# Kernel optimization log

Hardware: AMD Instinct MI355X
Metric: run time of the kernel (lower is better)

The kernel has to match this reference:

```python
import jax, jax.numpy as jnp
import numpy as np

B, H_, W_, C, HEADS, WS, SR = 4, 56, 56, 256, 8, 3, 4
HD = C // HEADS
N = H_ * W_
LL = WS * WS
PH, PW = H_ // SR, W_ // SR
PL = PH * PW
K_TAB = 2048


def _unfold3(x, H, W):
    # x: (B, C, H, W) -> (B, C, 9, H*W); matches torch nn.Unfold(kernel_size=3, padding=1)
    xp = jnp.pad(x, ((0, 0), (0, 0), (1, 1), (1, 1)))
    pats = jnp.stack([xp[:, :, i:i + H, j:j + W] for i in range(3) for j in range(3)], axis=2)
    return pats.reshape(x.shape[0], x.shape[1], 9, H * W)


def _l2n(x):
    # torch F.normalize(dim=-1) with eps=1e-12
    return x / jnp.maximum(jnp.linalg.norm(x, axis=-1, keepdims=True), 1e-12)


def setup_inputs() -> dict:
    key = jax.random.key(0)
    ks = jax.random.split(key, 24)
    x = jax.random.normal(ks[0], (B, N, C), jnp.float32)
    # padding mask from unfold of ones image (True where window element falls outside)
    ones = np.zeros((H_ + 2, W_ + 2), np.float32)
    ones[1:-1, 1:-1] = 1.0
    pats = np.stack([ones[i:i + H_, j:j + W_] for i in range(3) for j in range(3)], 0).reshape(9, N)
    padding_mask = jnp.asarray((pats == 0).T)  # (N, 9) bool
    local_valid = LL - padding_mask.sum(-1)
    seq_length_scale = jnp.log(local_valid.astype(jnp.float32) + PL)[:, None]  # (N,1)
    relative_pos_index = jax.random.randint(ks[1], (N * PL,), 0, K_TAB)
    relative_coords_table = jax.random.uniform(ks[2], (K_TAB, 2), jnp.float32, -1.0, 1.0)
    w = lambda k, shape: jax.random.normal(k, shape, jnp.float32) * 0.02
    inp = dict(
        x=x, H=H_, W=W_,
        relative_pos_index=relative_pos_index,
        relative_coords_table=relative_coords_table,
        seq_length_scale=seq_length_scale,
        padding_mask=padding_mask,
        q_w=w(ks[3], (C, C)), q_b=jnp.zeros((C,), jnp.float32),
        kv_w=w(ks[4], (2 * C, C)), kv_b=jnp.zeros((2 * C,), jnp.float32),
        sr_w=w(ks[5], (C, C)), sr_b=jnp.zeros((C,), jnp.float32),
        norm_g=jnp.ones((C,), jnp.float32), norm_b=jnp.zeros((C,), jnp.float32),
        cpb1_w=w(ks[6], (512, 2)), cpb1_b=jnp.zeros((512,), jnp.float32),
        cpb2_w=w(ks[7], (HEADS, 512)), cpb2_b=jnp.zeros((HEADS,), jnp.float32),
        temperature=jnp.log(jnp.exp(jnp.ones((HEADS, 1, 1), jnp.float32) / 0.24) - 1.0),
        query_embedding=w(ks[8], (HEADS, 1, HD)),
        rel_pos_bias_local=jax.random.normal(ks[9], (HEADS, LL), jnp.float32) * 0.0004,
        learnable_tokens=w(ks[10], (HEADS, HD, LL)),
        learnable_bias=jnp.zeros((HEADS, 1, LL), jnp.float32),
        proj_w=w(ks[11], (C, C)), proj_b=jnp.zeros((C,), jnp.float32),
    )
    return inp


def reference(x, H, W, relative_pos_index, relative_coords_table, seq_length_scale,
              padding_mask, q_w, q_b, kv_w, kv_b, sr_w, sr_b, norm_g, norm_b,
              cpb1_w, cpb1_b, cpb2_w, cpb2_b, temperature, query_embedding,
              rel_pos_bias_local, learnable_tokens, learnable_bias, proj_w, proj_b):
    Bsz, n, Cd = x.shape
    h, hd, ll = HEADS, HD, LL
    pH, pW = H // SR, W // SR
    pL = pH * pW
    # ----- queries -----
    q = (x @ q_w.T + q_b).reshape(Bsz, n, h, hd).transpose(0, 2, 1, 3)  # (B,h,N,d)
    q_norm = _l2n(q)
    q_scaled = (q_norm + query_embedding) * jax.nn.softplus(temperature) * seq_length_scale
    # ----- local branch: unfolded window KV -----
    kv = x @ kv_w.T + kv_b  # (B,N,2C)
    k_loc, v_loc = jnp.split(kv, 2, axis=-1)
    k_loc = _l2n(k_loc.reshape(Bsz, n, h, hd)).reshape(Bsz, n, Cd)
    kv_img = jnp.concatenate([k_loc, v_loc], -1).transpose(0, 2, 1).reshape(Bsz, 2 * Cd, H, W)
    pats = _unfold3(kv_img, H, W).reshape(Bsz, 2 * h, hd, ll, n).transpose(0, 1, 4, 2, 3)  # (B,2h,N,d,ll)
    k_local, v_local = jnp.split(pats, 2, axis=1)
    attn_local = jnp.einsum('bhnd,bhndl->bhnl', q_scaled, k_local) + rel_pos_bias_local[:, None, :]
    attn_local = jnp.where(padding_mask, -jnp.inf, attn_local)
    # ----- global branch: 1x1 conv -> GELU -> avg pool -> LN -> KV -----
    x_img = x.transpose(0, 2, 1).reshape(Bsz, Cd, H, W)
    x_sr = jax.nn.gelu(jnp.einsum('oc,bchw->bohw', sr_w, x_img) + sr_b[None, :, None, None], approximate=False)
    x_pool = x_sr.reshape(Bsz, Cd, pH, SR, pW, SR).mean(axis=(3, 5)).reshape(Bsz, Cd, pL).transpose(0, 2, 1)
    mu = x_pool.mean(-1, keepdims=True)
    var = x_pool.var(-1, keepdims=True)
    x_pool = (x_pool - mu) / jnp.sqrt(var + 1e-5) * norm_g + norm_b
    kvp = (x_pool @ kv_w.T + kv_b).reshape(Bsz, pL, 2 * h, hd).transpose(0, 2, 1, 3)
    k_pool, v_pool = jnp.split(kvp, 2, axis=1)  # each (B,h,pL,d)
    # CPB-MLP relative position bias (interpolate is identity since test==trained resolution)
    tab = jax.nn.relu(relative_coords_table @ cpb1_w.T + cpb1_b) @ cpb2_w.T + cpb2_b  # (K,h)
    pool_bias = tab.T[:, relative_pos_index].reshape(h, n, pL)
    attn_pool = jnp.einsum('bhnd,bhmd->bhnm', q_scaled, _l2n(k_pool)) + pool_bias
    # ----- joint softmax over [local | pool] -----
    attn = jax.nn.softmax(jnp.concatenate([attn_local, attn_pool], axis=-1), axis=-1)
    a_loc, a_pool = attn[..., :ll], attn[..., ll:]
    w_loc = jnp.einsum('bhnd,hdl->bhnl', q_norm, learnable_tokens) + learnable_bias + a_loc
    x_local = jnp.einsum('bhnl,bhndl->bhnd', w_loc, v_local)
    x_glob = jnp.einsum('bhnm,bhmd->bhnd', a_pool, v_pool)
    out = (x_local + x_glob).transpose(0, 2, 1, 3).reshape(Bsz, n, Cd)
    return out @ proj_w.T + proj_b
```

## Files before the change

### kernel.cpp

```cpp
#include <hip/hip_runtime.h>
#include <hip/hip_bf16.h>
#include <math.h>

#define Bn   4
#define Hh   56
#define Wn   56
#define Cn   256
#define NHn  8
#define HDn  32
#define Nn   3136
#define LLn  9
#define PLn  196
#define PWn  14
#define KTABn 2048
#define Mrows 12544
#define MP   224

#define XCNT   3211264
#define QWOFF  XCNT
#define KVWOFF (QWOFF + 65536)
#define SRWOFF (KVWOFF + 131072)
#define PWOFF  (SRWOFF + 65536)
#define TOTCVT (PWOFF + 65536)

typedef __attribute__((ext_vector_type(8))) short short8v;
typedef __attribute__((ext_vector_type(4))) float float4v;

__device__ __forceinline__ unsigned short f2b(float f) {
  __hip_bfloat16 h = __float2bfloat16(f);
  return *(unsigned short*)&h;
}
__device__ __forceinline__ float b2f(unsigned short u) {
  union { unsigned int i; float f; } x; x.i = ((unsigned int)u) << 16; return x.f;
}
__device__ __forceinline__ void u4_to8f(uint4 u, float* o) {
  o[0]=b2f((unsigned short)(u.x&0xffff)); o[1]=b2f((unsigned short)(u.x>>16));
  o[2]=b2f((unsigned short)(u.y&0xffff)); o[3]=b2f((unsigned short)(u.y>>16));
  o[4]=b2f((unsigned short)(u.z&0xffff)); o[5]=b2f((unsigned short)(u.z>>16));
  o[6]=b2f((unsigned short)(u.w&0xffff)); o[7]=b2f((unsigned short)(u.w>>16));
}

__launch_bounds__(256)
__global__ void cvt5(const float* __restrict__ x, const float* __restrict__ qw,
                     const float* __restrict__ kvw, const float* __restrict__ srw,
                     const float* __restrict__ pw, unsigned short* __restrict__ dst)
{
  const int i = (blockIdx.x * 256 + threadIdx.x) * 4;
  const float* src; int off;
  if      (i < XCNT)   { src = x;   off = 0; }
  else if (i < KVWOFF) { src = qw;  off = QWOFF; }
  else if (i < SRWOFF) { src = kvw; off = KVWOFF; }
  else if (i < PWOFF)  { src = srw; off = SRWOFF; }
  else                 { src = pw;  off = PWOFF; }
  const float4 v = *(const float4*)(src + (i - off));
  ushort4 o2;
  o2.x = f2b(v.x); o2.y = f2b(v.y); o2.z = f2b(v.z); o2.w = f2b(v.w);
  *(ushort4*)(dst + i) = o2;
}

template <int MODE>
__launch_bounds__(512)
__global__ void mgemm(const unsigned short* __restrict__ A,
                      const unsigned short* __restrict__ Wb,
                      const float* __restrict__ b0, const float* __restrict__ b1,
                      const float* __restrict__ b2, void* __restrict__ Cv, int Nc,
                      const float* __restrict__ sls, const float* __restrict__ qe,
                      const float* __restrict__ temp, float* __restrict__ Mq)
{
  __shared__ __align__(16) unsigned char smem[34816];
  unsigned short* As = (unsigned short*)smem;
  unsigned short* Bs = (unsigned short*)(smem + 16384);
  const int t = threadIdx.x;
  const int w = t >> 6, lane = t & 63;
  const int q = lane >> 4, ln = lane & 15;
  const int n0 = blockIdx.x * 128, m0 = blockIdx.y * 128;
  const int wm = (w >> 1) * 32, wn = (w & 1) * 64;

  float4v acc[2][4];
  #pragma unroll
  for (int mt = 0; mt < 2; ++mt)
    #pragma unroll
    for (int nt = 0; nt < 4; ++nt)
      acc[mt][nt] = (float4v){0.f, 0.f, 0.f, 0.f};

  for (int k0 = 0; k0 < 256; k0 += 64) {
    #pragma unroll
    for (int j = 0; j < 2; ++j) {
      const int u = t + 512 * j;
      const int r = u >> 3, cg = u & 7;
      const int cs = cg ^ (r & 7);
      const uint4 av = *(const uint4*)(A  + (size_t)(m0 + r) * 256 + k0 + cg * 8);
      *(uint4*)(As + r * 64 + cs * 8) = av;
      const uint4 bv = *(const uint4*)(Wb + (size_t)(n0 + r) * 256 + k0 + cg * 8);
      *(uint4*)(Bs + r * 64 + cs * 8) = bv;
    }
    __syncthreads();
    #pragma unroll
    for (int kk = 0; kk < 2; ++kk) {
      short8v af[2], bfr[4];
      const int cg = kk * 4 + q;
      #pragma unroll
      for (int mt = 0; mt < 2; ++mt) {
        const int r = wm + mt * 16 + ln;
        af[mt] = *(const short8v*)(As + r * 64 + (cg ^ (r & 7)) * 8);
      }
      #pragma unroll
      for (int nt = 0; nt < 4; ++nt) {
        const int r = wn + nt * 16 + ln;
        bfr[nt] = *(const short8v*)(Bs + r * 64 + (cg ^ (r & 7)) * 8);
      }
      #pragma unroll
      for (int mt = 0; mt < 2; ++mt)
        #pragma unroll
        for (int nt = 0; nt < 4; ++nt)
          acc[mt][nt] = __builtin_amdgcn_mfma_f32_16x16x32_bf16(af[mt], bfr[nt], acc[mt][nt], 0, 0, 0);
    }
    __syncthreads();
  }

  if constexpr (MODE == 0) {
    float* C = (float*)Cv;
    float* tileF = (float*)smem;
    float bia[4];
    #pragma unroll
    for (int nt = 0; nt < 4; ++nt) bia[nt] = b0[n0 + wn + nt * 16 + ln];
    #pragma unroll
    for (int half = 0; half < 2; ++half) {
      if ((w >> 2) == half) {
        #pragma unroll
        for (int mt = 0; mt < 2; ++mt)
          #pragma unroll
          for (int r = 0; r < 4; ++r)
            #pragma unroll
            for (int nt = 0; nt < 4; ++nt)
              tileF[(wm - half*64 + mt*16 + q*4 + r) * 132 + wn + nt*16 + ln] = acc[mt][nt][r] + bia[nt];
      }
      __syncthreads();
      #pragma unroll
      for (int j = 0; j < 4; ++j) {
        const int i = j * 512 + t;
        const int row = i >> 5, ch = i & 31;
        float4 v = *(const float4*)(tileF + row * 132 + ch * 4);
        *(float4*)(C + (size_t)(m0 + half * 64 + row) * Nc + n0 + ch * 4) = v;
      }
      __syncthreads();
    }
  } else {
    unsigned short* Cb = (unsigned short*)Cv;
    unsigned short* tileC = (unsigned short*)smem;
    const int seg = n0 >> 8;
    const int h0 = (n0 + wn) >> 5, h1 = h0 + 1;
    float spt0 = 0.f, spt1 = 0.f;
    if (seg == 0) { spt0 = log1pf(__expf(temp[h0])); spt1 = log1pf(__expf(temp[h1])); }
    float bia[4], qev[4];
    #pragma unroll
    for (int nt = 0; nt < 4; ++nt) {
      const int col = n0 + wn + nt * 16 + ln;
      bia[nt] = (seg == 0) ? b0[col] : (seg == 3 ? b2[col - 768] : b1[col - 256]);
      if (seg == 0) qev[nt] = qe[col];
    }
    #pragma unroll
    for (int mt = 0; mt < 2; ++mt) {
      #pragma unroll
      for (int r = 0; r < 4; ++r) {
        const int row = m0 + wm + mt * 16 + q * 4 + r;
        const int lrow = wm + mt * 16 + q * 4 + r;
        float vals[4];
        #pragma unroll
        for (int nt = 0; nt < 4; ++nt) vals[nt] = acc[mt][nt][r] + bia[nt];
        if (seg == 0) {
          float ss0 = vals[0]*vals[0] + vals[1]*vals[1];
          float ss1 = vals[2]*vals[2] + vals[3]*vals[3];
          #pragma unroll
          for (int mk = 1; mk <= 8; mk <<= 1) { ss0 += __shfl_xor(ss0, mk); ss1 += __shfl_xor(ss1, mk); }
          const float i0 = 1.f / fmaxf(sqrtf(ss0), 1e-12f);
          const float i1 = 1.f / fmaxf(sqrtf(ss1), 1e-12f);
          const int nidx = row % Nn, bb = row / Nn;
          const float sl = sls[nidx];
          float qsv[4];
          #pragma unroll
          for (int nt = 0; nt < 4; ++nt) {
            const float inv = (nt < 2) ? i0 : i1;
            const float sp  = (nt < 2) ? spt0 : spt1;
            qsv[nt] = (vals[nt] * inv + qev[nt]) * sp * sl;
          }
          float t0 = qsv[0]*qsv[0] + qsv[1]*qsv[1];
          float t1 = qsv[2]*qsv[2] + qsv[3]*qsv[3];
          #pragma unroll
          for (int mk = 1; mk <= 8; mk <<= 1) { t0 += __shfl_xor(t0, mk); t1 += __shfl_xor(t1, mk); }
          if (ln == 0) {
            Mq[((size_t)(bb * NHn + h0)) * Nn + nidx] = sqrtf(t0);
            Mq[((size_t)(bb * NHn + h1)) * Nn + nidx] = sqrtf(t1);
          }
          #pragma unroll
          for (int nt = 0; nt < 4; ++nt)
            tileC[lrow * 136 + wn + nt*16 + ln] = f2b(qsv[nt]);
        } else if (seg == 1) {
          float ss0 = vals[0]*vals[0] + vals[1]*vals[1];
          float ss1 = vals[2]*vals[2] + vals[3]*vals[3];
          #pragma unroll
          for (int mk = 1; mk <= 8; mk <<= 1) { ss0 += __shfl_xor(ss0, mk); ss1 += __shfl_xor(ss1, mk); }
          const float i0 = 1.f / fmaxf(sqrtf(ss0), 1e-12f);
          const float i1 = 1.f / fmaxf(sqrtf(ss1), 1e-12f);
          #pragma unroll
          for (int nt = 0; nt < 4; ++nt)
            tileC[lrow * 136 + wn + nt*16 + ln] = f2b(vals[nt] * ((nt < 2) ? i0 : i1));
        } else if (seg == 2) {
          #pragma unroll
          for (int nt = 0; nt < 4; ++nt)
            tileC[lrow * 136 + wn + nt*16 + ln] = f2b(vals[nt]);
        } else {
          #pragma unroll
          for (int nt = 0; nt < 4; ++nt) {
            const float v = vals[nt];
            tileC[lrow * 136 + wn + nt*16 + ln] =
              f2b(0.5f * v * (1.0f + erff(v * 0.70710678118654752f)));
          }
        }
      }
    }
    __syncthreads();
    #pragma unroll
    for (int j = 0; j < 4; ++j) {
      const int i = j * 512 + t;
      const int row = i >> 4, ch = i & 15;
      uint4 v = *(const uint4*)(tileC + row * 136 + ch * 8);
      *(uint4*)(Cb + (size_t)(m0 + row) * 1024 + n0 + ch * 8) = v;
    }
  }
}

__launch_bounds__(256)
__global__ void gemm_k(const float* __restrict__ A, const float* __restrict__ W,
                       const float* __restrict__ bias, float* __restrict__ Co,
                       int Mr, int Nc, int K)
{
  __shared__ __align__(16) float As[16][64];
  __shared__ __align__(16) float Ws[16][64];
  const int t  = threadIdx.x;
  const int m0 = blockIdx.y * 64, n0 = blockIdx.x * 64;
  const int lm = t >> 2, lk = (t & 3) << 2;
  const int tx = t & 15, ty = t >> 4;
  float acc[4][4] = {};
  int arow = m0 + lm; if (arow >= Mr) arow = Mr - 1;
  const int wrow = n0 + lm;
  for (int k0 = 0; k0 < K; k0 += 16) {
    float4 av = *(const float4*)(A + (size_t)arow * K + k0 + lk);
    As[lk+0][lm] = av.x; As[lk+1][lm] = av.y; As[lk+2][lm] = av.z; As[lk+3][lm] = av.w;
    float4 wv = *(const float4*)(W + (size_t)wrow * K + k0 + lk);
    Ws[lk+0][lm] = wv.x; Ws[lk+1][lm] = wv.y; Ws[lk+2][lm] = wv.z; Ws[lk+3][lm] = wv.w;
    __syncthreads();
    #pragma unroll
    for (int k = 0; k < 16; ++k) {
      float4 a = *(const float4*)&As[k][ty << 2];
      float4 w = *(const float4*)&Ws[k][tx << 2];
      acc[0][0] += a.x*w.x; acc[0][1] += a.x*w.y; acc[0][2] += a.x*w.z; acc[0][3] += a.x*w.w;
      acc[1][0] += a.y*w.x; acc[1][1] += a.y*w.y; acc[1][2] += a.y*w.z; acc[1][3] += a.y*w.w;
      acc[2][0] += a.z*w.x; acc[2][1] += a.z*w.y; acc[2][2] += a.z*w.z; acc[2][3] += a.z*w.w;
      acc[3][0] += a.w*w.x; acc[3][1] += a.w*w.y; acc[3][2] += a.w*w.z; acc[3][3] += a.w*w.w;
    }
    __syncthreads();
  }
  #pragma unroll
  for (int i = 0; i < 4; ++i) {
    const int row = m0 + (ty << 2) + i;
    if (row >= Mr) continue;
    #pragma unroll
    for (int j = 0; j < 4; ++j) {
      const int col = n0 + (tx << 2) + j;
      Co[(size_t)row * Nc + col] = acc[i][j] + bias[col];
    }
  }
}

__launch_bounds__(256)
__global__ void pool_ln_k(const unsigned short* __restrict__ fused, float* __restrict__ pln,
                          const float* __restrict__ g, const float* __restrict__ bb)
{
  const int blk = blockIdx.x;
  const int b = blk / PLn, pc = blk % PLn;
  const int pi = pc / PWn, pj = pc % PWn;
  const int c = threadIdx.x;
  float s = 0.f;
  #pragma unroll
  for (int r = 0; r < 4; ++r)
    #pragma unroll
    for (int cc = 0; cc < 4; ++cc) {
      const int n = (pi*4 + r) * Wn + pj*4 + cc;
      s += b2f(fused[((size_t)b * Nn + n) * 1024 + 768 + c]);
    }
  s *= (1.f/16.f);
  float sum = s, sq = s*s;
  #pragma unroll
  for (int m = 32; m >= 1; m >>= 1) { sum += __shfl_xor(sum, m); sq += __shfl_xor(sq, m); }
  __shared__ float sm[8];
  const int lane = c & 63, wid = c >> 6;
  if (lane == 0) { sm[wid] = sum; sm[4+wid] = sq; }
  __syncthreads();
  const float tot  = sm[0]+sm[1]+sm[2]+sm[3];
  const float totq = sm[4]+sm[5]+sm[6]+sm[7];
  const float mu  = tot * (1.f/256.f);
  const float var = totq * (1.f/256.f) - mu*mu;
  pln[(size_t)blk * Cn + c] = (s - mu) / sqrtf(var + 1e-5f) * g[c] + bb[c];
}

__launch_bounds__(256)
__global__ void pool_pack(const float* __restrict__ kvp, unsigned short* __restrict__ kbf,
                          unsigned short* __restrict__ vbf)
{
  const int bh = blockIdx.x;
  const int b = bh >> 3, h = bh & 7;
  const int t = threadIdx.x, mg = t >> 5, d = t & 31;
  for (int mi = 0; mi < MP/8; ++mi) {
    const int m = mi * 8 + mg;
    float kv2 = 0.f, vv = 0.f;
    if (m < PLn) {
      kv2 = kvp[((size_t)(b * PLn + m)) * 512 + h * HDn + d];
      vv  = kvp[((size_t)(b * PLn + m)) * 512 + 256 + h * HDn + d];
    }
    float ssn = kv2 * kv2;
    #pragma unroll
    for (int mm = 16; mm >= 1; mm >>= 1) ssn += __shfl_xor(ssn, mm);
    const float kn = (m < PLn) ? kv2 / fmaxf(sqrtf(ssn), 1e-12f) : 0.f;
    kbf[((size_t)bh * MP + m) * HDn + d] = f2b(kn);
    vbf[((size_t)bh * 32 + d) * MP + m] = f2b(vv);
  }
}

__launch_bounds__(64)
__global__ void cpb_k(const float* __restrict__ rct, const float* __restrict__ w1,
                      const float* __restrict__ b1, const float* __restrict__ w2,
                      const float* __restrict__ b2, float* __restrict__ tab)
{
  const int r = blockIdx.x, t = threadIdx.x;
  const float c0 = rct[r*2], c1 = rct[r*2+1];
  float part[8] = {};
  #pragma unroll
  for (int jj = 0; jj < 8; ++jj) {
    const int j = t * 8 + jj;
    float hv = fmaxf(c0 * w1[j*2] + c1 * w1[j*2+1] + b1[j], 0.f);
    #pragma unroll
    for (int h = 0; h < 8; ++h) part[h] += hv * w2[h*512 + j];
  }
  #pragma unroll
  for (int h = 0; h < 8; ++h)
    for (int mm = 32; mm >= 1; mm >>= 1) part[h] += __shfl_xor(part[h], mm);
  if (t < 8) tab[r*8 + t] = part[t] + b2[t];
}

__launch_bounds__(256)
__global__ void redmax_k(const float* __restrict__ tab, const float* __restrict__ rpb,
                         float* __restrict__ scal)
{
  float mx = -1e30f;
  for (int i = threadIdx.x; i < KTABn*NHn; i += 256) mx = fmaxf(mx, tab[i]);
  if (threadIdx.x < NHn*LLn) mx = fmaxf(mx, rpb[threadIdx.x]);
  #pragma unroll
  for (int m = 32; m >= 1; m >>= 1) mx = fmaxf(mx, __shfl_xor(mx, m));
  __shared__ float sm[4];
  if ((threadIdx.x & 63) == 0) sm[threadIdx.x >> 6] = mx;
  __syncthreads();
  if (threadIdx.x == 0) scal[0] = fmaxf(fmaxf(sm[0], sm[1]), fmaxf(sm[2], sm[3]));
}

__launch_bounds__(256)
__global__ void bias_g2(const int* __restrict__ rpi, const float* __restrict__ tab,
                        unsigned short* __restrict__ bias2)
{
  const int mt = blockIdx.x, nt = blockIdx.y;
  const int t = threadIdx.x;
  const int nn = t >> 4, mm = t & 15;
  const int n = nt * 16 + nn, m = mt * 16 + mm;
  unsigned short vh[NHn];
  if (m < PLn) {
    const int idx = rpi[(size_t)n * PLn + m];
    #pragma unroll
    for (int h = 0; h < NHn; ++h) vh[h] = f2b(tab[(size_t)idx * NHn + h]);
  } else {
    #pragma unroll
    for (int h = 0; h < NHn; ++h) vh[h] = 0xFF80;
  }
  #pragma unroll
  for (int h = 0; h < NHn; ++h)
    bias2[(((size_t)h * 196 + nt) * 14 + mt) * 256 + t] = vh[h];
}

__launch_bounds__(256)
__global__ void attn_f(const unsigned short* __restrict__ fused,
                       const unsigned short* __restrict__ kbf,
                       const unsigned short* __restrict__ vbf,
                       const unsigned short* __restrict__ bias2,
                       const float* __restrict__ Mq, const float* __restrict__ scal,
                       const float* __restrict__ slsp, const float* __restrict__ temp,
                       const float* __restrict__ qe, const float* __restrict__ lt,
                       const float* __restrict__ lb, const float* __restrict__ rpb,
                       unsigned short* __restrict__ outp)
{
  __shared__ __align__(16) unsigned short sh[21888];
  unsigned short* k_s   = sh;
  unsigned short* v_s   = sh + 7200;
  unsigned short* p_lds = sh + 14400;
  float* park = (float*)(sh + 16960);
  float* tabf = (float*)(sh + 21184);
  float* qe_s  = tabf;
  float* lt_s  = tabf + 32;
  float* lb_s  = tabf + 320;
  float* rpb_s = tabf + 329;
  const int t = threadIdx.x;
  const int w = t >> 6, lane = t & 63;
  const int ln = lane & 15, quad = lane >> 4;
  const int tile = blockIdx.x, h = blockIdx.y, b = blockIdx.z;
  const int bh = b * NHn + h;

  if (t < 32) qe_s[t] = qe[h * HDn + t];
  for (int i = t; i < HDn * LLn; i += 256) lt_s[i] = lt[h * HDn * LLn + i];
  if (t < LLn) { lb_s[t] = lb[h * LLn + t]; rpb_s[t] = rpb[h * LLn + t]; }
  const int base_n = tile * 64 - 57;
  for (int i = t; i < 720; i += 256) {
    const int row = i >> 2, c4 = i & 3;
    int rg = base_n + row; rg = rg < 0 ? 0 : (rg > Nn - 1 ? Nn - 1 : rg);
    const unsigned short* src = fused + ((size_t)(b * Nn + rg)) * 1024 + 256 + h * HDn + c4 * 8;
    *(uint4*)(k_s + row * 40 + c4 * 8) = *(const uint4*)src;
    *(uint4*)(v_s + row * 40 + c4 * 8) = *(const uint4*)(src + 256);
  }
  __syncthreads();

  const int nb = tile * 64 + w * 16;
  const short8v afrag = *(const short8v*)(fused +
      ((size_t)(b * Nn + nb + ln)) * 1024 + h * HDn + quad * 8);
  float M4[4];
  const float sc = scal[0];
  #pragma unroll
  for (int r = 0; r < 4; ++r) M4[r] = Mq[(size_t)bh * Nn + nb + quad * 4 + r] + sc;

  const unsigned short* kg = kbf + (size_t)bh * (MP * HDn);
  const unsigned short* vg = vbf + (size_t)bh * (32 * MP);
  const unsigned short* b2t = bias2 + (((size_t)h * 196 + (tile * 4 + w)) * 14) * 256;
  unsigned short* pst = p_lds + w * 640;

  float4v accO[2];
  accO[0] = (float4v){0.f,0.f,0.f,0.f};
  accO[1] = (float4v){0.f,0.f,0.f,0.f};
  float lsum[4] = {0.f, 0.f, 0.f, 0.f};

  #pragma unroll
  for (int kc = 0; kc < 7; ++kc) {
    #pragma unroll
    for (int mtl = 0; mtl < 2; ++mtl) {
      const int mt = kc * 2 + mtl;
      short8v bfrag = *(const short8v*)(kg + (mt * 16 + ln) * HDn + quad * 8);
      float4v s = __builtin_amdgcn_mfma_f32_16x16x32_bf16(afrag, bfrag,
                                                          (float4v){0.f,0.f,0.f,0.f}, 0, 0, 0);
      #pragma unroll
      for (int r = 0; r < 4; ++r) {
        const float bv = b2f(b2t[mt * 256 + (quad * 4 + r) * 16 + ln]);
        const float p = __expf(s[r] + bv - M4[r]);
        const unsigned short pb = f2b(p);
        lsum[r] += b2f(pb);
        pst[(quad * 4 + r) * 40 + mtl * 16 + ln] = pb;
      }
    }
    short8v pa = *(const short8v*)(pst + ln * 40 + quad * 8);
    #pragma unroll
    for (int nt = 0; nt < 2; ++nt) {
      short8v vb = *(const short8v*)(vg + (size_t)(nt * 16 + ln) * MP + kc * 32 + quad * 8);
      accO[nt] = __builtin_amdgcn_mfma_f32_16x16x32_bf16(pa, vb, accO[nt], 0, 0, 0);
    }
  }

  #pragma unroll
  for (int r = 0; r < 4; ++r) {
    #pragma unroll
    for (int mk = 1; mk <= 8; mk <<= 1) lsum[r] += __shfl_xor(lsum[r], mk);
  }

  float* mypark = park + w * 528;
  #pragma unroll
  for (int r = 0; r < 4; ++r) {
    const int row = quad * 4 + r;
    mypark[row * 33 + ln]      = accO[0][r];
    mypark[row * 33 + 16 + ln] = accO[1][r];
    if (ln == 0) mypark[row * 33 + 32] = lsum[r];
  }

  const int nl = t >> 2, dg = t & 3;
  const int n = tile * 64 + nl;
  float qs8[8];
  u4_to8f(*(const uint4*)(fused + ((size_t)(b * Nn + n)) * 1024 + h * HDn + dg * 8), qs8);
  const float M = Mq[(size_t)bh * Nn + n] + sc;
  const float spt = log1pf(__expf(temp[h]));
  const float inv_qs = 1.f / (spt * slsp[n]);

  float acc8[8], ext8[8];
  #pragma unroll
  for (int j = 0; j < 8; ++j) { acc8[j] = 0.f; ext8[j] = 0.f; }
  float l_run = 0.f;
  const int pi = n / Wn, pj = n % Wn;
  const int sb = nl + 57;
  #pragma unroll
  for (int lc = 0; lc < LLn; ++lc) {
    const int ii = pi + lc/3 - 1, jj = pj + (lc%3) - 1;
    if (ii < 0 || ii >= Hh || jj < 0 || jj >= Wn) continue;
    const int slot = sb + (lc/3 - 1) * 56 + (lc%3) - 1;
    float kk8[8], vv8[8];
    u4_to8f(*(const uint4*)(k_s + slot * 40 + dg * 8), kk8);
    u4_to8f(*(const uint4*)(v_s + slot * 40 + dg * 8), vv8);
    float pp = 0.f, ep = 0.f;
    #pragma unroll
    for (int j = 0; j < 8; ++j) {
      pp += qs8[j] * kk8[j];
      ep += (qs8[j] * inv_qs - qe_s[dg*8 + j]) * lt_s[(dg*8 + j) * LLn + lc];
    }
    pp += __shfl_xor(pp, 1); pp += __shfl_xor(pp, 2);
    ep += __shfl_xor(ep, 1); ep += __shfl_xor(ep, 2);
    const float e = ep + lb_s[lc];
    const float p = __expf(pp + rpb_s[lc] - M);
    l_run += p;
    #pragma unroll
    for (int j = 0; j < 8; ++j) { acc8[j] += p * vv8[j]; ext8[j] += e * vv8[j]; }
  }

  const float* pool_r = park + w * 528 + (nl - w * 16) * 33;
  const float l_pool = pool_r[32];
  const float invl = 1.f / (l_run + l_pool);
  uint4 u;
  {
    const float* op = pool_r + dg * 8;
    float o0 = (acc8[0]+op[0])*invl + ext8[0], o1 = (acc8[1]+op[1])*invl + ext8[1];
    float o2 = (acc8[2]+op[2])*invl + ext8[2], o3 = (acc8[3]+op[3])*invl + ext8[3];
    float o4 = (acc8[4]+op[4])*invl + ext8[4], o5 = (acc8[5]+op[5])*invl + ext8[5];
    float o6 = (acc8[6]+op[6])*invl + ext8[6], o7 = (acc8[7]+op[7])*invl + ext8[7];
    u.x = f2b(o0) | ((unsigned int)f2b(o1) << 16);
    u.y = f2b(o2) | ((unsigned int)f2b(o3) << 16);
    u.z = f2b(o4) | ((unsigned int)f2b(o5) << 16);
    u.w = f2b(o6) | ((unsigned int)f2b(o7) << 16);
  }
  *(uint4*)(outp + ((size_t)b * Nn + n) * Cn + h * HDn + dg * 8) = u;
}

extern "C" void kernel_launch(void* const* d_in, const int* in_sizes, int n_in,
                              void* d_out, int out_size, void* d_ws, size_t ws_size,
                              hipStream_t stream)
{
  const float* x    = (const float*)d_in[0];
  const int*   rpi  = (const int*)d_in[3];
  const float* rct  = (const float*)d_in[4];
  const float* sls  = (const float*)d_in[5];
  const float* q_w  = (const float*)d_in[7];
  const float* q_b  = (const float*)d_in[8];
  const float* kv_w = (const float*)d_in[9];
  const float* kv_b = (const float*)d_in[10];
  const float* sr_w = (const float*)d_in[11];
  const float* sr_b = (const float*)d_in[12];
  const float* ng   = (const float*)d_in[13];
  const float* nbta = (const float*)d_in[14];
  const float* c1w  = (const float*)d_in[15];
  const float* c1b  = (const float*)d_in[16];
  const float* c2w  = (const float*)d_in[17];
  const float* c2b  = (const float*)d_in[18];
  const float* temp = (const float*)d_in[19];
  const float* qe   = (const float*)d_in[20];
  const float* rpb  = (const float*)d_in[21];
  const float* lt   = (const float*)d_in[22];
  const float* lb   = (const float*)d_in[23];
  const float* pw   = (const float*)d_in[24];
  const float* pb   = (const float*)d_in[25];

  float* ws = (float*)d_ws;
  size_t o = 0;
  unsigned short* bf = (unsigned short*)(ws + o); o += TOTCVT / 2;
  unsigned short* fused = (unsigned short*)(ws + o); o += (size_t)Mrows * 512;
  float* Mq    = ws + o;  o += (size_t)Bn * NHn * Nn;
  float* pln   = ws + o;  o += (size_t)Bn * PLn * Cn;
  float* kvp   = ws + o;  o += (size_t)Bn * PLn * 2 * Cn;
  unsigned short* kbf = (unsigned short*)(ws + o); o += (size_t)Bn * NHn * MP * HDn / 2;
  unsigned short* vbf = (unsigned short*)(ws + o); o += (size_t)Bn * NHn * 32 * MP / 2;
  float* tab   = ws + o;  o += (size_t)KTABn * NHn;
  float* scal  = ws + o;  o += 8;
  unsigned short* bias2 = (unsigned short*)(ws + o); o += (size_t)NHn * Nn * MP / 2;
  unsigned short* outp  = (unsigned short*)(ws + o); o += (size_t)Mrows * Cn / 2;

  const unsigned short* xbf   = bf;
  const unsigned short* qkvsw = bf + QWOFF;
  const unsigned short* pwbf  = bf + PWOFF;

  cvt5<<<TOTCVT/1024, 256, 0, stream>>>(x, q_w, kv_w, sr_w, pw, bf);
  mgemm<1><<<dim3(8, 98), 512, 0, stream>>>(xbf, qkvsw, q_b, kv_b, sr_b, fused, 1024,
                                            sls, qe, temp, Mq);
  pool_ln_k<<<Bn*PLn, 256, 0, stream>>>(fused, pln, ng, nbta);
  gemm_k<<<dim3(8, 13), 256, 0, stream>>>(pln, kv_w, kv_b, kvp, Bn*PLn, 512, 256);
  pool_pack<<<Bn*NHn, 256, 0, stream>>>(kvp, kbf, vbf);
  cpb_k<<<KTABn, 64, 0, stream>>>(rct, c1w, c1b, c2w, c2b, tab);
  redmax_k<<<1, 256, 0, stream>>>(tab, rpb, scal);
  bias_g2<<<dim3(14, 196), 256, 0, stream>>>(rpi, tab, bias2);
  attn_f<<<dim3(49, NHn, Bn), 256, 0, stream>>>(fused, kbf, vbf, bias2, Mq, scal,
                                                sls, temp, qe, lt, lb, rpb, outp);
  mgemm<0><<<dim3(2, 98), 512, 0, stream>>>(outp, pwbf, pb, pb, pb, (float*)d_out, 256,
                                            nullptr, nullptr, nullptr, nullptr);
}
```

Before: 251.2 us.

## Repack pool bias per lane for register preload and widen small prep kernels

The gathered relative-position bias is rewritten into a per-lane layout that holds 16 consecutive m-tile values, so attn_f loads each row's bias once into registers with vector loads. This replaces the scattered per-element global loads inside the softmax loop. The LDS footprint of attn_f is trimmed and launch_bounds now requests 4 blocks per SM for higher occupancy. pool_pack is split across 7 y-blocks and redmax runs with 1024 threads to parallelise those small serial kernels, at the cost of a larger padded bias buffer and extra register pressure.

```diff
diff --git a/kernel.cpp b/kernel.cpp
--- a/kernel.cpp
+++ b/kernel.cpp
@@ -311,7 +311,8 @@
   const int bh = blockIdx.x;
   const int b = bh >> 3, h = bh & 7;
   const int t = threadIdx.x, mg = t >> 5, d = t & 31;
-  for (int mi = 0; mi < MP/8; ++mi) {
+  const int mi0 = blockIdx.y * 4;
+  for (int mi = mi0; mi < mi0 + 4; ++mi) {
     const int m = mi * 8 + mg;
     float kv2 = 0.f, vv = 0.f;
     if (m < PLn) {
@@ -348,44 +349,53 @@
   if (t < 8) tab[r*8 + t] = part[t] + b2[t];
 }
 
-__launch_bounds__(256)
+__launch_bounds__(1024)
 __global__ void redmax_k(const float* __restrict__ tab, const float* __restrict__ rpb,
                          float* __restrict__ scal)
 {
   float mx = -1e30f;
-  for (int i = threadIdx.x; i < KTABn*NHn; i += 256) mx = fmaxf(mx, tab[i]);
+  for (int i = threadIdx.x; i < KTABn*NHn; i += 1024) mx = fmaxf(mx, tab[i]);
   if (threadIdx.x < NHn*LLn) mx = fmaxf(mx, rpb[threadIdx.x]);
   #pragma unroll
   for (int m = 32; m >= 1; m >>= 1) mx = fmaxf(mx, __shfl_xor(mx, m));
-  __shared__ float sm[4];
+  __shared__ float sm[16];
   if ((threadIdx.x & 63) == 0) sm[threadIdx.x >> 6] = mx;
   __syncthreads();
-  if (threadIdx.x == 0) scal[0] = fmaxf(fmaxf(sm[0], sm[1]), fmaxf(sm[2], sm[3]));
+  if (threadIdx.x == 0) {
+    float m2 = sm[0];
+    #pragma unroll
+    for (int i = 1; i < 16; ++i) m2 = fmaxf(m2, sm[i]);
+    scal[0] = m2;
+  }
 }
 
 __launch_bounds__(256)
 __global__ void bias_g2(const int* __restrict__ rpi, const float* __restrict__ tab,
                         unsigned short* __restrict__ bias2)
 {
-  const int mt = blockIdx.x, nt = blockIdx.y;
+  const int nt = blockIdx.x, h = blockIdx.y;
   const int t = threadIdx.x;
-  const int nn = t >> 4, mm = t & 15;
-  const int n = nt * 16 + nn, m = mt * 16 + mm;
-  unsigned short vh[NHn];
-  if (m < PLn) {
-    const int idx = rpi[(size_t)n * PLn + m];
-    #pragma unroll
-    for (int h = 0; h < NHn; ++h) vh[h] = f2b(tab[(size_t)idx * NHn + h]);
-  } else {
-    #pragma unroll
-    for (int h = 0; h < NHn; ++h) vh[h] = 0xFF80;
-  }
-  #pragma unroll
-  for (int h = 0; h < NHn; ++h)
-    bias2[(((size_t)h * 196 + nt) * 14 + mt) * 256 + t] = vh[h];
-}
-
-__launch_bounds__(256)
+  const int row = t >> 4, ln = t & 15;
+  const int n = nt * 16 + row;
+  union { uint4 u[2]; unsigned short s[16]; } pk;
+  #pragma unroll
+  for (int mt = 0; mt < 16; ++mt) {
+    const int m = mt * 16 + ln;
+    unsigned short v;
+    if (mt < 14 && m < PLn) {
+      const int idx = rpi[(size_t)n * PLn + m];
+      v = f2b(tab[(size_t)idx * NHn + h]);
+    } else {
+      v = 0xFF80;
+    }
+    pk.s[mt] = v;
+  }
+  unsigned short* dst = bias2 + ((((size_t)h * 196 + nt) * 256 + t) << 4);
+  *(uint4*)dst = pk.u[0];
+  *(uint4*)(dst + 8) = pk.u[1];
+}
+
+__launch_bounds__(256, 4)
 __global__ void attn_f(const unsigned short* __restrict__ fused,
                        const unsigned short* __restrict__ kbf,
                        const unsigned short* __restrict__ vbf,
@@ -396,12 +406,11 @@
                        const float* __restrict__ lb, const float* __restrict__ rpb,
                        unsigned short* __restrict__ outp)
 {
-  __shared__ __align__(16) unsigned short sh[21888];
-  unsigned short* k_s   = sh;
-  unsigned short* v_s   = sh + 7200;
-  unsigned short* p_lds = sh + 14400;
-  float* park = (float*)(sh + 16960);
-  float* tabf = (float*)(sh + 21184);
+  __shared__ __align__(16) unsigned short sh[19140];
+  unsigned short* k_s = sh;
+  unsigned short* v_s = sh + 7120;
+  float* park = (float*)(sh + 14240);
+  float* tabf = (float*)(sh + 18464);
   float* qe_s  = tabf;
   float* lt_s  = tabf + 32;
   float* lb_s  = tabf + 320;
@@ -416,7 +425,7 @@
   for (int i = t; i < HDn * LLn; i += 256) lt_s[i] = lt[h * HDn * LLn + i];
   if (t < LLn) { lb_s[t] = lb[h * LLn + t]; rpb_s[t] = rpb[h * LLn + t]; }
   const int base_n = tile * 64 - 57;
-  for (int i = t; i < 720; i += 256) {
+  for (int i = t; i < 712; i += 256) {
     const int row = i >> 2, c4 = i & 3;
     int rg = base_n + row; rg = rg < 0 ? 0 : (rg > Nn - 1 ? Nn - 1 : rg);
     const unsigned short* src = fused + ((size_t)(b * Nn + rg)) * 1024 + 256 + h * HDn + c4 * 8;
@@ -426,6 +435,7 @@
   __syncthreads();
 
   const int nb = tile * 64 + w * 16;
+  const int nt2 = tile * 4 + w;
   const short8v afrag = *(const short8v*)(fused +
       ((size_t)(b * Nn + nb + ln)) * 1024 + h * HDn + quad * 8);
   float M4[4];
@@ -433,10 +443,19 @@
   #pragma unroll
   for (int r = 0; r < 4; ++r) M4[r] = Mq[(size_t)bh * Nn + nb + quad * 4 + r] + sc;
 
+  union U16 { uint4 u[2]; unsigned short s[16]; };
+  U16 breg[4];
+  #pragma unroll
+  for (int r = 0; r < 4; ++r) {
+    const unsigned short* bp = bias2 +
+        ((((size_t)h * 196 + nt2) * 256 + (quad * 4 + r) * 16 + ln) << 4);
+    breg[r].u[0] = *(const uint4*)bp;
+    breg[r].u[1] = *(const uint4*)(bp + 8);
+  }
+
   const unsigned short* kg = kbf + (size_t)bh * (MP * HDn);
   const unsigned short* vg = vbf + (size_t)bh * (32 * MP);
-  const unsigned short* b2t = bias2 + (((size_t)h * 196 + (tile * 4 + w)) * 14) * 256;
-  unsigned short* pst = p_lds + w * 640;
+  unsigned short* pst = sh + 14240 + w * 1056;
 
   float4v accO[2];
   accO[0] = (float4v){0.f,0.f,0.f,0.f};
@@ -453,7 +472,7 @@
                                                           (float4v){0.f,0.f,0.f,0.f}, 0, 0, 0);
       #pragma unroll
       for (int r = 0; r < 4; ++r) {
-        const float bv = b2f(b2t[mt * 256 + (quad * 4 + r) * 16 + ln]);
+        const float bv = b2f(breg[r].s[mt]);
         const float p = __expf(s[r] + bv - M4[r]);
         const unsigned short pb = f2b(p);
         lsum[r] += b2f(pb);
@@ -577,7 +596,7 @@
   unsigned short* vbf = (unsigned short*)(ws + o); o += (size_t)Bn * NHn * 32 * MP / 2;
   float* tab   = ws + o;  o += (size_t)KTABn * NHn;
   float* scal  = ws + o;  o += 8;
-  unsigned short* bias2 = (unsigned short*)(ws + o); o += (size_t)NHn * Nn * MP / 2;
+  unsigned short* bias2 = (unsigned short*)(ws + o); o += (size_t)NHn * 196 * 256 * 16 / 2;
   unsigned short* outp  = (unsigned short*)(ws + o); o += (size_t)Mrows * Cn / 2;
 
   const unsigned short* xbf   = bf;
@@ -589,10 +608,10 @@
                                             sls, qe, temp, Mq);
   pool_ln_k<<<Bn*PLn, 256, 0, stream>>>(fused, pln, ng, nbta);
   gemm_k<<<dim3(8, 13), 256, 0, stream>>>(pln, kv_w, kv_b, kvp, Bn*PLn, 512, 256);
-  pool_pack<<<Bn*NHn, 256, 0, stream>>>(kvp, kbf, vbf);
+  pool_pack<<<dim3(Bn*NHn, 7), 256, 0, stream>>>(kvp, kbf, vbf);
   cpb_k<<<KTABn, 64, 0, stream>>>(rct, c1w, c1b, c2w, c2b, tab);
-  redmax_k<<<1, 256, 0, stream>>>(tab, rpb, scal);
-  bias_g2<<<dim3(14, 196), 256, 0, stream>>>(rpi, tab, bias2);
+  redmax_k<<<1, 1024, 0, stream>>>(tab, rpb, scal);
+  bias_g2<<<dim3(196, NHn), 256, 0, stream>>>(rpi, tab, bias2);
   attn_f<<<dim3(49, NHn, Bn), 256, 0, stream>>>(fused, kbf, vbf, bias2, Mq, scal,
                                                 sls, temp, qe, lt, lb, rpb, outp);
   mgemm<0><<<dim3(2, 98), 512, 0, stream>>>(outp, pwbf, pb, pb, pb, (float*)d_out, 256,
```

Result: faster. 239.0 us (-4.9%).
